# Kernel tuning notes

Measured on AMD Instinct MI355X. Metric: run time of the kernel, lower is better.

The kernel has to match this reference:

```python
import jax, jax.numpy as jnp
import numpy as np

# EISANI constants (inference path, dense non-EI weights, static connections)
NUM_BITS = 16        # EISANITABcontinuousVarEncodingNumBits
K_SYN = 32           # numberOfSynapsesPerSegment
SEGMENTS = 2         # numberOfSegmentsPerNeuron
THETA = 8            # segment activation threshold (synapse-count based)
H = 4096             # hiddenLayerSize
F = 128              # numberOfFeatures
C = 10               # numberOfClasses
B = 64               # batch


def _make_weight(key, h, s, p):
    """Dense weight [h, s, p] with exactly K_SYN nonzero +/-1 synapses per segment
    (mirrors _initialise_layer_weights dense non-EI branch)."""
    k1, k2 = jax.random.split(key)
    cols = jax.random.randint(k1, (h, s, K_SYN), 0, p)
    signs = jnp.where(jax.random.bernoulli(k2, 0.5, (h, s, K_SYN)), 1.0, -1.0).astype(jnp.float32)
    hh = jnp.arange(h)[:, None, None]
    ss = jnp.arange(s)[None, :, None]
    return jnp.zeros((h, s, p), jnp.float32).at[hh, ss, cols].set(signs)


def setup_inputs() -> dict:
    key = jax.random.key(0)
    kx, k0, k1, k2, ko = jax.random.split(key, 5)
    x = jax.random.uniform(kx, (B, F), dtype=jnp.float32)
    W0 = _make_weight(k0, H, SEGMENTS, F * NUM_BITS)
    W1 = _make_weight(k1, H, SEGMENTS, H)
    W2 = _make_weight(k2, H, SEGMENTS, H)
    outW = jax.random.normal(ko, (3, H, C), dtype=jnp.float32) * 0.02
    return {"x": x, "W0": W0, "W1": W1, "W2": W2, "outW": outW}


def _encode(x):
    # thermometer (graded) encoding of continuous vars into NUM_BITS binary bits
    thresholds = (jnp.arange(NUM_BITS, dtype=jnp.float32) + 1.0) / (NUM_BITS + 1.0)
    bits = (x[:, :, None] >= thresholds).astype(jnp.float32)  # [B, F, NUM_BITS]
    return bits.reshape(x.shape[0], -1)  # [B, F*NUM_BITS]


def reference(x, W0, W1, W2, outW):
    acts = _encode(x)  # [B, P0]
    layer_acts = []
    for W in (W0, W1, W2):
        # segment membrane sums over binary presynaptic activations
        z = jnp.einsum('bp,hsp->bhs', acts, W)  # [B, H, S]
        # neuron fires if ANY segment reaches threshold
        fired = jnp.any(z >= THETA, axis=-1)
        acts = fired.astype(jnp.float32)  # binary activation [B, H]
        layer_acts.append(acts)
    stacked = jnp.stack(layer_acts)  # [L, B, H]
    out = jnp.einsum('lbh,lhc->bc', stacked, outW)  # class scores [B, C]
    return out
```

## Files before the change

kernel.cpp:

```cpp
#include <hip/hip_runtime.h>
#include <hip/hip_bf16.h>

typedef unsigned long long u64;
typedef float f32x4 __attribute__((ext_vector_type(4)));

#define H_SZ 4096
#define NBITS 16
#define NFEAT 128
#define NCLS 10
#define THETA 8


__global__ void encode_kernel(const float* __restrict__ x, u64* __restrict__ actp0) {
    int idx = blockIdx.x * blockDim.x + threadIdx.x;
    if (idx >= 32 * 64) return;
    int wword = idx >> 6;
    int b = idx & 63;
    int c = wword >> 2, j = wword & 3;
    float thr0 = (4 * 0 + j + 1.0f) / (NBITS + 1.0f);
    float thr1 = (4 * 1 + j + 1.0f) / (NBITS + 1.0f);
    float thr2 = (4 * 2 + j + 1.0f) / (NBITS + 1.0f);
    float thr3 = (4 * 3 + j + 1.0f) / (NBITS + 1.0f);
    const float* xb = x + b * NFEAT + c * 16;
    u64 word = 0;
    #pragma unroll
    for (int k = 0; k < 16; k++) {
        float xv = xb[k];
        word |= (u64)(xv >= thr0) << (4 * k + 0);
        word |= (u64)(xv >= thr1) << (4 * k + 1);
        word |= (u64)(xv >= thr2) << (4 * k + 2);
        word |= (u64)(xv >= thr3) << (4 * k + 3);
    }
    actp0[wword * 64 + b] = word;
}

template <int P>
__global__ __launch_bounds__(256, 4) void layer_kernel(const float* __restrict__ W,
                                                       const u64* __restrict__ actp,
                                                       u64* __restrict__ ballots) {
    constexpr int NW = P / 64;
    __shared__ __align__(16) u64 lds[NW * 64];
    int tid = threadIdx.x;
    const ulonglong2* src = (const ulonglong2*)actp;
    ulonglong2* dst = (ulonglong2*)lds;
    #pragma unroll
    for (int i = tid; i < NW * 32; i += 256) dst[i] = src[i];
    __syncthreads();

    int lane = tid & 63;
    int warp = tid >> 6;
    int wid0 = (blockIdx.x * 4 + warp) * 2;
    const f32x4* w0 = (const f32x4*)(W + (size_t)wid0 * P) + lane;
    const f32x4* w1 = (const f32x4*)(W + (size_t)(wid0 + 1) * P) + lane;

    unsigned int zp0 = 0, zn0 = 0, zp1 = 0, zn1 = 0;
    #pragma unroll 4
    for (int c = 0; c < P / 256; c++) {
        f32x4 a = __builtin_nontemporal_load(w0 + c * 64);
        f32x4 b = __builtin_nontemporal_load(w1 + c * 64);
        u64 A0 = lds[(c * 4 + 0) * 64 + lane];
        u64 A1 = lds[(c * 4 + 1) * 64 + lane];
        u64 A2 = lds[(c * 4 + 2) * 64 + lane];
        u64 A3 = lds[(c * 4 + 3) * 64 + lane];

        u64 m;
        m = __ballot(a.x > 0.0f); zp0 += __builtin_popcountll(A0 & m);
        m = __ballot(a.x < 0.0f); zn0 += __builtin_popcountll(A0 & m);
        m = __ballot(a.y > 0.0f); zp0 += __builtin_popcountll(A1 & m);
        m = __ballot(a.y < 0.0f); zn0 += __builtin_popcountll(A1 & m);
        m = __ballot(a.z > 0.0f); zp0 += __builtin_popcountll(A2 & m);
        m = __ballot(a.z < 0.0f); zn0 += __builtin_popcountll(A2 & m);
        m = __ballot(a.w > 0.0f); zp0 += __builtin_popcountll(A3 & m);
        m = __ballot(a.w < 0.0f); zn0 += __builtin_popcountll(A3 & m);

        m = __ballot(b.x > 0.0f); zp1 += __builtin_popcountll(A0 & m);
        m = __ballot(b.x < 0.0f); zn1 += __builtin_popcountll(A0 & m);
        m = __ballot(b.y > 0.0f); zp1 += __builtin_popcountll(A1 & m);
        m = __ballot(b.y < 0.0f); zn1 += __builtin_popcountll(A1 & m);
        m = __ballot(b.z > 0.0f); zp1 += __builtin_popcountll(A2 & m);
        m = __ballot(b.z < 0.0f); zn1 += __builtin_popcountll(A2 & m);
        m = __ballot(b.w > 0.0f); zp1 += __builtin_popcountll(A3 & m);
        m = __ballot(b.w < 0.0f); zn1 += __builtin_popcountll(A3 & m);
    }
    int z0 = (int)zp0 - (int)zn0;
    int z1 = (int)zp1 - (int)zn1;
    u64 f0 = __ballot(z0 >= THETA);
    u64 f1 = __ballot(z1 >= THETA);
    if (lane == 0) {
        ballots[wid0] = f0;
        ballots[wid0 + 1] = f1;
    }
}

__global__ void transpose_kernel(const u64* __restrict__ ballots,
                                 u64* __restrict__ f,
                                 u64* __restrict__ actp) {
    __shared__ u64 lds[256];
    int c = blockIdx.x;
    int tid = threadIdx.x;
    int h = c * 256 + tid;
    u64 fh = ballots[2 * h] | ballots[2 * h + 1];
    f[h] = fh;
    lds[tid] = fh;
    __syncthreads();
    int j = tid >> 6, b = tid & 63;
    u64 word = 0;
    #pragma unroll 8
    for (int i = 0; i < 64; i++)
        word |= ((lds[4 * i + j] >> b) & 1ULL) << i;
    actp[(c * 4 + j) * 64 + b] = word;
}

__global__ void output_kernel(const float* __restrict__ outW,
                              const u64* __restrict__ f,
                              const u64* __restrict__ ballots,
                              float* __restrict__ out) {
    int tid = threadIdx.x;
    int lane = tid & 63;
    int wid = blockIdx.x * 4 + (tid >> 6);
    int l = wid / (NCLS * 64);
    int rem = wid % (NCLS * 64);
    int c = rem / 64;
    int chunk = rem % 64;
    int h0 = chunk * 64;
    float acc = 0.0f;
    if (l < 2) {
        const u64* fl = f + l * H_SZ;
        #pragma unroll 8
        for (int h = h0; h < h0 + 64; h++) {
            float wv = outW[((size_t)(l * H_SZ + h)) * NCLS + c];
            if ((fl[h] >> lane) & 1ULL) acc += wv;
        }
    } else {
        #pragma unroll 8
        for (int h = h0; h < h0 + 64; h++) {
            float wv = outW[((size_t)(2 * H_SZ + h)) * NCLS + c];
            u64 ball = ballots[2 * h] | ballots[2 * h + 1];
            if ((ball >> lane) & 1ULL) acc += wv;
        }
    }
    atomicAdd(&out[lane * NCLS + c], acc);
}

extern "C" void kernel_launch(void* const* d_in, const int* in_sizes, int n_in,
                              void* d_out, int out_size, void* d_ws, size_t ws_size,
                              hipStream_t stream) {
    const float* x    = (const float*)d_in[0];
    const float* W0   = (const float*)d_in[1];
    const float* W1   = (const float*)d_in[2];
    const float* W2   = (const float*)d_in[3];
    const float* outW = (const float*)d_in[4];
    float* out = (float*)d_out;

    char* ws = (char*)d_ws;
    u64* actp0   = (u64*)(ws);
    u64* actp1   = (u64*)(ws + 16384);
    u64* actp2   = (u64*)(ws + 49152);
    u64* ballots = (u64*)(ws + 81920);
    u64* f       = (u64*)(ws + 147456);

    hipMemsetAsync(d_out, 0, (size_t)out_size * sizeof(float), stream);

    encode_kernel<<<8, 256, 0, stream>>>(x, actp0);

    layer_kernel<2048><<<1024, 256, 0, stream>>>(W0, actp0, ballots);
    transpose_kernel<<<16, 256, 0, stream>>>(ballots, f + 0 * H_SZ, actp1);

    layer_kernel<4096><<<1024, 256, 0, stream>>>(W1, actp1, ballots);
    transpose_kernel<<<16, 256, 0, stream>>>(ballots, f + 1 * H_SZ, actp2);

    layer_kernel<4096><<<1024, 256, 0, stream>>>(W2, actp2, ballots);

    output_kernel<<<480, 256, 0, stream>>>(outW, f, ballots, out);
}
```

Measured before the change: 365.7 us.

## Fuse bit transpose into layer kernel and prefetch weights before LDS fill

Result: faster. 342.8 us (-6.3%).

```diff
diff --git a/kernel.cpp b/kernel.cpp
--- a/kernel.cpp
+++ b/kernel.cpp
@@ -34,35 +34,64 @@
     actp0[wword * 64 + b] = word;
 }
 
-template <int P>
+__device__ __forceinline__ u64 bfly_stage(u64 x, int lane, int d, u64 Md) {
+    u64 p = __shfl_xor(x, d);
+    return (lane & d) ? ((x & Md) | ((p >> d) & ~Md))
+                      : ((x & ~Md) | ((p << d) & Md));
+}
+
+__device__ __forceinline__ u64 transpose64(u64 x, int lane) {
+    x = bfly_stage(x, lane, 32, 0xFFFFFFFF00000000ULL);
+    x = bfly_stage(x, lane, 16, 0xFFFF0000FFFF0000ULL);
+    x = bfly_stage(x, lane,  8, 0xFF00FF00FF00FF00ULL);
+    x = bfly_stage(x, lane,  4, 0xF0F0F0F0F0F0F0F0ULL);
+    x = bfly_stage(x, lane,  2, 0xCCCCCCCCCCCCCCCCULL);
+    x = bfly_stage(x, lane,  1, 0xAAAAAAAAAAAAAAAAULL);
+    return x;
+}
+
+template <int P, bool FROM_FIRED>
 __global__ __launch_bounds__(256, 4) void layer_kernel(const float* __restrict__ W,
-                                                       const u64* __restrict__ actp,
-                                                       u64* __restrict__ ballots) {
+                                                       const u64* __restrict__ actin,
+                                                       u64* __restrict__ fired_out) {
     constexpr int NW = P / 64;
+    constexpr int NC = P / 256;
     __shared__ __align__(16) u64 lds[NW * 64];
     int tid = threadIdx.x;
-    const ulonglong2* src = (const ulonglong2*)actp;
-    ulonglong2* dst = (ulonglong2*)lds;
+    int lane = tid & 63;
+    int warp = tid >> 6;
+    int h = blockIdx.x * 4 + warp;
+    const f32x4* w0 = (const f32x4*)(W + (size_t)(2 * h) * P) + lane;
+    const f32x4* w1 = (const f32x4*)(W + (size_t)(2 * h + 1) * P) + lane;
+
+    f32x4 pa[4], pb[4];
     #pragma unroll
-    for (int i = tid; i < NW * 32; i += 256) dst[i] = src[i];
+    for (int c = 0; c < 4; c++) {
+        pa[c] = __builtin_nontemporal_load(w0 + c * 64);
+        pb[c] = __builtin_nontemporal_load(w1 + c * 64);
+    }
+
+    if constexpr (FROM_FIRED) {
+        #pragma unroll 4
+        for (int c = 0; c < 16; c++) {
+            u64 xw = actin[c * 256 + 4 * lane + warp];
+            xw = transpose64(xw, lane);
+            lds[(c * 4 + warp) * 64 + lane] = xw;
+        }
+    } else {
+        const ulonglong2* src = (const ulonglong2*)actin;
+        ulonglong2* dst = (ulonglong2*)lds;
+        #pragma unroll
+        for (int i = tid; i < NW * 32; i += 256) dst[i] = src[i];
+    }
     __syncthreads();
 
-    int lane = tid & 63;
-    int warp = tid >> 6;
-    int wid0 = (blockIdx.x * 4 + warp) * 2;
-    const f32x4* w0 = (const f32x4*)(W + (size_t)wid0 * P) + lane;
-    const f32x4* w1 = (const f32x4*)(W + (size_t)(wid0 + 1) * P) + lane;
-
     unsigned int zp0 = 0, zn0 = 0, zp1 = 0, zn1 = 0;
-    #pragma unroll 4
-    for (int c = 0; c < P / 256; c++) {
-        f32x4 a = __builtin_nontemporal_load(w0 + c * 64);
-        f32x4 b = __builtin_nontemporal_load(w1 + c * 64);
+    auto body = [&](int c, f32x4 a, f32x4 b) {
         u64 A0 = lds[(c * 4 + 0) * 64 + lane];
         u64 A1 = lds[(c * 4 + 1) * 64 + lane];
         u64 A2 = lds[(c * 4 + 2) * 64 + lane];
         u64 A3 = lds[(c * 4 + 3) * 64 + lane];
-
         u64 m;
         m = __ballot(a.x > 0.0f); zp0 += __builtin_popcountll(A0 & m);
         m = __ballot(a.x < 0.0f); zn0 += __builtin_popcountll(A0 & m);
@@ -81,65 +110,50 @@
         m = __ballot(b.z < 0.0f); zn1 += __builtin_popcountll(A2 & m);
         m = __ballot(b.w > 0.0f); zp1 += __builtin_popcountll(A3 & m);
         m = __ballot(b.w < 0.0f); zn1 += __builtin_popcountll(A3 & m);
+    };
+
+    #pragma unroll
+    for (int c = 0; c < 4; c++) body(c, pa[c], pb[c]);
+    #pragma unroll 4
+    for (int c = 4; c < NC; c++) {
+        f32x4 a = __builtin_nontemporal_load(w0 + c * 64);
+        f32x4 b = __builtin_nontemporal_load(w1 + c * 64);
+        body(c, a, b);
     }
+
     int z0 = (int)zp0 - (int)zn0;
     int z1 = (int)zp1 - (int)zn1;
     u64 f0 = __ballot(z0 >= THETA);
     u64 f1 = __ballot(z1 >= THETA);
-    if (lane == 0) {
-        ballots[wid0] = f0;
-        ballots[wid0 + 1] = f1;
-    }
-}
-
-__global__ void transpose_kernel(const u64* __restrict__ ballots,
-                                 u64* __restrict__ f,
-                                 u64* __restrict__ actp) {
-    __shared__ u64 lds[256];
-    int c = blockIdx.x;
-    int tid = threadIdx.x;
-    int h = c * 256 + tid;
-    u64 fh = ballots[2 * h] | ballots[2 * h + 1];
-    f[h] = fh;
-    lds[tid] = fh;
-    __syncthreads();
-    int j = tid >> 6, b = tid & 63;
-    u64 word = 0;
-    #pragma unroll 8
-    for (int i = 0; i < 64; i++)
-        word |= ((lds[4 * i + j] >> b) & 1ULL) << i;
-    actp[(c * 4 + j) * 64 + b] = word;
+    if (lane == 0) fired_out[h] = f0 | f1;
 }
 
 __global__ void output_kernel(const float* __restrict__ outW,
-                              const u64* __restrict__ f,
-                              const u64* __restrict__ ballots,
+                              const u64* __restrict__ fired,
                               float* __restrict__ out) {
+    __shared__ float red[4][64];
     int tid = threadIdx.x;
     int lane = tid & 63;
-    int wid = blockIdx.x * 4 + (tid >> 6);
+    int warp = tid >> 6;
+    int wid = blockIdx.x * 4 + warp;
     int l = wid / (NCLS * 64);
     int rem = wid % (NCLS * 64);
     int c = rem / 64;
     int chunk = rem % 64;
+    const u64* fl = fired + l * H_SZ;
     int h0 = chunk * 64;
     float acc = 0.0f;
-    if (l < 2) {
-        const u64* fl = f + l * H_SZ;
-        #pragma unroll 8
-        for (int h = h0; h < h0 + 64; h++) {
-            float wv = outW[((size_t)(l * H_SZ + h)) * NCLS + c];
-            if ((fl[h] >> lane) & 1ULL) acc += wv;
-        }
-    } else {
-        #pragma unroll 8
-        for (int h = h0; h < h0 + 64; h++) {
-            float wv = outW[((size_t)(2 * H_SZ + h)) * NCLS + c];
-            u64 ball = ballots[2 * h] | ballots[2 * h + 1];
-            if ((ball >> lane) & 1ULL) acc += wv;
-        }
+    #pragma unroll 8
+    for (int h = h0; h < h0 + 64; h++) {
+        float wv = outW[((size_t)(l * H_SZ + h)) * NCLS + c];
+        if ((fl[h] >> lane) & 1ULL) acc += wv;
     }
-    atomicAdd(&out[lane * NCLS + c], acc);
+    red[warp][lane] = acc;
+    __syncthreads();
+    if (warp == 0) {
+        float s = red[0][lane] + red[1][lane] + red[2][lane] + red[3][lane];
+        atomicAdd(&out[lane * NCLS + c], s);
+    }
 }
 
 extern "C" void kernel_launch(void* const* d_in, const int* in_sizes, int n_in,
@@ -153,23 +167,16 @@
     float* out = (float*)d_out;
 
     char* ws = (char*)d_ws;
-    u64* actp0   = (u64*)(ws);
-    u64* actp1   = (u64*)(ws + 16384);
-    u64* actp2   = (u64*)(ws + 49152);
-    u64* ballots = (u64*)(ws + 81920);
-    u64* f       = (u64*)(ws + 147456);
+    u64* actp0 = (u64*)(ws);
+    u64* fired = (u64*)(ws + 16384);
 
     hipMemsetAsync(d_out, 0, (size_t)out_size * sizeof(float), stream);
 
     encode_kernel<<<8, 256, 0, stream>>>(x, actp0);
 
-    layer_kernel<2048><<<1024, 256, 0, stream>>>(W0, actp0, ballots);
-    transpose_kernel<<<16, 256, 0, stream>>>(ballots, f + 0 * H_SZ, actp1);
+    layer_kernel<2048, false><<<1024, 256, 0, stream>>>(W0, actp0, fired + 0 * H_SZ);
+    layer_kernel<4096, true ><<<1024, 256, 0, stream>>>(W1, fired + 0 * H_SZ, fired + 1 * H_SZ);
+    layer_kernel<4096, true ><<<1024, 256, 0, stream>>>(W2, fired + 1 * H_SZ, fired + 2 * H_SZ);
 
-    layer_kernel<4096><<<1024, 256, 0, stream>>>(W1, actp1, ballots);
-    transpose_kernel<<<16, 256, 0, stream>>>(ballots, f + 1 * H_SZ, actp2);
-
-    layer_kernel<4096><<<1024, 256, 0, stream>>>(W2, actp2, ballots);
-
-    output_kernel<<<480, 256, 0, stream>>>(outW, f, ballots, out);
+    output_kernel<<<480, 256, 0, stream>>>(outW, fired, out);
 }
```
